# Optimization experiments

Hardware: AMD Instinct MI355X
Metric: run time of the kernel (lower is better)

Reference implementation:

```python
import jax, jax.numpy as jnp
import numpy as np

N, L, G = 8192, 120, 256          # sentences, seq_len, bags
V, P = 80000, 202                 # word vocab, position vocab
WDIM, FDIM = 50, 5                # word_size, feature_size (width = 50+2*5 = 60)
D, C = 230, 53                    # cnn_layers, num_classes


def setup_inputs() -> dict:
    key = jax.random.key(0)
    ks = jax.random.split(key, 9)
    x = jax.random.randint(ks[0], (N, L), 0, V, dtype=jnp.int32)
    ldist = jax.random.randint(ks[1], (N, L), 0, P, dtype=jnp.int32)
    rdist = jax.random.randint(ks[2], (N, L), 0, P, dtype=jnp.int32)
    # cumulative bag boundaries: 256 equal bags of 32 sentences
    total_shape = (jnp.arange(G + 1, dtype=jnp.int32) * (N // G))
    Wv = jax.random.normal(ks[3], (V, WDIM), dtype=jnp.float32) * 0.1
    pf1 = jax.random.normal(ks[4], (P, FDIM), dtype=jnp.float32) * 0.1
    pf2 = jax.random.normal(ks[5], (P, FDIM), dtype=jnp.float32) * 0.1
    Wc = jax.random.normal(ks[6], (D, 1, 3, WDIM + 2 * FDIM), dtype=jnp.float32) * 0.05
    bc = jnp.zeros((D,), dtype=jnp.float32)
    Wr = jax.random.normal(ks[7], (C, D), dtype=jnp.float32) * 0.05
    br = jnp.zeros((C,), dtype=jnp.float32)
    return dict(x=x, ldist=ldist, rdist=rdist, total_shape=total_shape,
                Wv=Wv, pf1=pf1, pf2=pf2, Wc=Wc, bc=bc, Wr=Wr, br=br)


def reference(x, ldist, rdist, total_shape, Wv, pf1, pf2, Wc, bc, Wr, br):
    n = x.shape[0]
    g = total_shape.shape[0] - 1
    # getEmbeddings: concat word + two position embeddings -> (N, L, 60)
    emb = jnp.concatenate([Wv[x], pf1[ldist], pf2[rdist]], axis=-1)
    # Conv2d(1, D, (3, 60)), VALID -> (N, D, L-2, 1)
    conv = jax.lax.conv_general_dilated(
        emb[:, None, :, :], Wc, window_strides=(1, 1), padding='VALID',
        dimension_numbers=('NCHW', 'OIHW', 'NCHW')) + bc[None, :, None, None]
    # max over positions, squeeze; dropout is identity at eval; tanh
    sent = jnp.tanh(jnp.max(conv, axis=2)[:, :, 0])           # (N, D)
    e = sent @ Wr.T + br                                       # (N, C) batch_e
    # ragged per-bag softmax over sentences (per class), honoring total_shape
    seg = jnp.searchsorted(total_shape, jnp.arange(n), side='right') - 1  # (N,)
    m = jax.ops.segment_max(e, seg, num_segments=g)            # (G, C)
    ex = jnp.exp(e - m[seg])
    den = jax.ops.segment_sum(ex, seg, num_segments=g)
    alpha = ex / den[seg]                                      # (N, C)
    # bag_rep[g, c, :] = sum_i alpha[i, c] * sent[i, :]
    bag = jax.ops.segment_sum(alpha[:, :, None] * sent[:, None, :], seg,
                              num_segments=g)                  # (G, C, D)
    scores = jnp.einsum('gcd,kd->gck', bag, Wr) + br           # (G, C, C)
    probs = jax.nn.softmax(scores, axis=-1)
    return jnp.diagonal(probs, axis1=1, axis2=2)               # (G, C)
```

## Files before the change

### kernel.cpp

```cpp
#include <hip/hip_runtime.h>
#include <hip/hip_bf16.h>

typedef __bf16 bf16x8 __attribute__((ext_vector_type(8)));
typedef float f32x16 __attribute__((ext_vector_type(16)));
typedef unsigned short ushort_t;

#define NSENT 8192
#define LSEQ  120
#define GBAGS 256
#define WDIM_ 50
#define DFILT 230
#define NCLS  53
#define KSTEPS 12
#define BFRAG_ELEMS (24*256*8)
#define LROWS 130
#define SPB 4

static __device__ __forceinline__ ushort_t f2bf(float f) {
    unsigned int u = __float_as_uint(f);
    unsigned int lsb = (u >> 16) & 1u;
    u += 0x7fffu + lsb;
    return (ushort_t)(u >> 16);
}

__global__ __launch_bounds__(256) void pcnn_prep_b(const float* __restrict__ Wc,
                                                   ushort_t* __restrict__ Bfrag) {
    int idx = blockIdx.x * 256 + threadIdx.x;
    if (idx >= BFRAG_ELEMS) return;
    int c   = idx >> 11;
    int rem = idx & 2047;
    int d   = rem >> 3;
    int j   = rem & 7;
    int k   = c * 8 + j;
    int dh  = k >> 6;
    int w   = k & 63;
    float val = (d < DFILT && w < 60) ? Wc[(d * 3 + dh) * 60 + w] : 0.0f;
    Bfrag[idx] = f2bf(val);
}

__device__ __forceinline__ void conv_gather(unsigned char* __restrict__ buf, int n,
    const int* __restrict__ x, const int* __restrict__ ld, const int* __restrict__ rd,
    const float* __restrict__ Wv, const float* __restrict__ pf1, const float* __restrict__ pf2,
    int tid) {
    if (tid >= 240) return;
    int l = tid >> 1, h = tid & 1;
    int tok = x[n * LSEQ + l];
    float v[32];
    const float* wr = Wv + tok * WDIM_;
    if (h == 0) {
        #pragma unroll
        for (int j = 0; j < 16; ++j) {
            float2 t2 = *reinterpret_cast<const float2*>(wr + 2 * j);
            v[2 * j] = t2.x; v[2 * j + 1] = t2.y;
        }
    } else {
        #pragma unroll
        for (int j = 0; j < 9; ++j) {
            float2 t2 = *reinterpret_cast<const float2*>(wr + 32 + 2 * j);
            v[2 * j] = t2.x; v[2 * j + 1] = t2.y;
        }
        int lp = ld[n * LSEQ + l], rp = rd[n * LSEQ + l];
        #pragma unroll
        for (int j = 0; j < 5; ++j) v[18 + j] = pf1[lp * 5 + j];
        #pragma unroll
        for (int j = 0; j < 5; ++j) v[23 + j] = pf2[rp * 5 + j];
        v[28] = v[29] = v[30] = v[31] = 0.0f;
    }
    #pragma unroll
    for (int ch = 0; ch < 4; ++ch) {
        ushort_t u8[8];
        #pragma unroll
        for (int j = 0; j < 8; ++j) u8[j] = f2bf(v[ch * 8 + j]);
        int w0 = h * 32 + ch * 8;
        int byteoff = l * 128 + ((w0 * 2) ^ ((l & 7) << 4));
        *reinterpret_cast<uint4*>(buf + byteoff) = *reinterpret_cast<const uint4*>(u8);
    }
}

__device__ __forceinline__ void conv_compute(const unsigned char* __restrict__ buf, int n,
    const bf16x8 (&Bf)[2][KSTEPS], const float* __restrict__ bc, float* __restrict__ sent,
    int wv, int lhalf, int l31) {
    float dmax0 = -1e30f, dmax1 = -1e30f;
    #pragma unroll
    for (int tt = 0; tt < 4; ++tt) {
        f32x16 acc0, acc1;
        #pragma unroll
        for (int r = 0; r < 16; ++r) { acc0[r] = 0.0f; acc1[r] = 0.0f; }
        int trow = tt * 32 + l31;
        #pragma unroll
        for (int ks = 0; ks < KSTEPS; ++ks) {
            int dh = ks >> 2, q = ks & 3;
            int l = trow + dh;
            int w0 = q * 16 + lhalf * 8;
            int byteoff = l * 128 + ((w0 * 2) ^ ((l & 7) << 4));
            bf16x8 Af = *reinterpret_cast<const bf16x8*>(buf + byteoff);
            acc0 = __builtin_amdgcn_mfma_f32_32x32x16_bf16(Af, Bf[0][ks], acc0, 0, 0, 0);
            acc1 = __builtin_amdgcn_mfma_f32_32x32x16_bf16(Af, Bf[1][ks], acc1, 0, 0, 0);
        }
        #pragma unroll
        for (int r = 0; r < 16; ++r) {
            int t = tt * 32 + (r & 3) + 8 * (r >> 2) + 4 * lhalf;
            bool valid = (tt < 3) || (t < LSEQ - 2);
            if (valid) { dmax0 = fmaxf(dmax0, acc0[r]); dmax1 = fmaxf(dmax1, acc1[r]); }
        }
    }
    dmax0 = fmaxf(dmax0, __shfl_xor(dmax0, 32));
    dmax1 = fmaxf(dmax1, __shfl_xor(dmax1, 32));
    if (lhalf == 0) {
        int d0 = (wv * 2 + 0) * 32 + l31;
        int d1 = (wv * 2 + 1) * 32 + l31;
        if (d0 < DFILT) sent[n * DFILT + d0] = tanhf(dmax0 + bc[d0]);
        if (d1 < DFILT) sent[n * DFILT + d1] = tanhf(dmax1 + bc[d1]);
    }
}

__global__ __launch_bounds__(256) void pcnn_conv_sent(
    const int* __restrict__ x, const int* __restrict__ ld, const int* __restrict__ rd,
    const float* __restrict__ Wv, const float* __restrict__ pf1, const float* __restrict__ pf2,
    const ushort_t* __restrict__ Bfrag, const float* __restrict__ bc,
    float* __restrict__ sent) {

    __shared__ __align__(16) unsigned char sembA[LROWS * 128];
    __shared__ __align__(16) unsigned char sembB[LROWS * 128];

    const int n0   = blockIdx.x * SPB;
    const int tid  = threadIdx.x;
    const int wv   = tid >> 6;
    const int lane = tid & 63;
    const int lhalf = lane >> 5;
    const int l31   = lane & 31;

    bf16x8 Bf[2][KSTEPS];
    #pragma unroll
    for (int i = 0; i < 2; ++i) {
        int dcol = (wv * 2 + i) * 32 + l31;
        #pragma unroll
        for (int ks = 0; ks < KSTEPS; ++ks) {
            int c = ks * 2 + lhalf;
            Bf[i][ks] = *reinterpret_cast<const bf16x8*>(Bfrag + ((c * 256 + dcol) << 3));
        }
    }

    if (tid < 160) {
        int b = tid / 80, j = tid % 80;
        unsigned char* base = (b == 0 ? sembA : sembB) + 120 * 128;
        reinterpret_cast<uint4*>(base)[j] = uint4{0, 0, 0, 0};
    }
    conv_gather(sembA, n0 + 0, x, ld, rd, Wv, pf1, pf2, tid);
    __syncthreads();

    conv_gather(sembB, n0 + 1, x, ld, rd, Wv, pf1, pf2, tid);
    conv_compute(sembA, n0 + 0, Bf, bc, sent, wv, lhalf, l31);
    __syncthreads();
    conv_gather(sembA, n0 + 2, x, ld, rd, Wv, pf1, pf2, tid);
    conv_compute(sembB, n0 + 1, Bf, bc, sent, wv, lhalf, l31);
    __syncthreads();
    conv_gather(sembB, n0 + 3, x, ld, rd, Wv, pf1, pf2, tid);
    conv_compute(sembA, n0 + 2, Bf, bc, sent, wv, lhalf, l31);
    __syncthreads();
    conv_compute(sembB, n0 + 3, Bf, bc, sent, wv, lhalf, l31);
}

#define MAXNS 32
#define CPAD 56
__global__ __launch_bounds__(256) void pcnn_bag(
    const float* __restrict__ sent, const float* __restrict__ Wr, const float* __restrict__ br,
    const int* __restrict__ tshape, float* __restrict__ out) {

    __shared__ float s_sent[MAXNS * DFILT];
    __shared__ float s_Wr[NCLS * DFILT];
    __shared__ float s_e[MAXNS * CPAD];
    __shared__ float s_alpha[MAXNS * CPAD];
    __shared__ float s_sc[NCLS * NCLS];
    __shared__ float s_br[CPAD];

    const int g = blockIdx.x;
    const int tid = threadIdx.x;
    int start = tshape[g], end = tshape[g + 1];
    int ns = end - start;
    if (ns > MAXNS) ns = MAXNS;

    {
        int n2 = ns * (DFILT / 2);
        const float2* src = reinterpret_cast<const float2*>(sent + start * DFILT);
        for (int idx = tid; idx < n2; idx += 256)
            reinterpret_cast<float2*>(s_sent)[idx] = src[idx];
        const float2* wsrc = reinterpret_cast<const float2*>(Wr);
        for (int idx = tid; idx < (NCLS * DFILT) / 2; idx += 256)
            reinterpret_cast<float2*>(s_Wr)[idx] = wsrc[idx];
        if (tid < NCLS) s_br[tid] = br[tid];
    }
    __syncthreads();

    if (tid < 224) {
        int i0 = tid / 14, c0 = tid % 14;
        float a00 = 0, a01 = 0, a02 = 0, a03 = 0;
        float a10 = 0, a11 = 0, a12 = 0, a13 = 0;
        const float* s0p = s_sent + (2 * i0) * DFILT;
        const float* s1p = s_sent + (2 * i0 + 1) * DFILT;
        const float* w0p = s_Wr + (4 * c0 + 0) * DFILT;
        const float* w1p = s_Wr + (4 * c0 + 1) * DFILT;
        const float* w2p = (4 * c0 + 2 < NCLS) ? s_Wr + (4 * c0 + 2) * DFILT : s_Wr;
        const float* w3p = (4 * c0 + 3 < NCLS) ? s_Wr + (4 * c0 + 3) * DFILT : s_Wr;
        for (int d = 0; d < DFILT; ++d) {
            float s0 = s0p[d], s1 = s1p[d];
            float w0 = w0p[d], w1 = w1p[d], w2 = w2p[d], w3 = w3p[d];
            a00 = fmaf(s0, w0, a00); a01 = fmaf(s0, w1, a01);
            a02 = fmaf(s0, w2, a02); a03 = fmaf(s0, w3, a03);
            a10 = fmaf(s1, w0, a10); a11 = fmaf(s1, w1, a11);
            a12 = fmaf(s1, w2, a12); a13 = fmaf(s1, w3, a13);
        }
        float av[2][4] = {{a00, a01, a02, a03}, {a10, a11, a12, a13}};
        #pragma unroll
        for (int ii = 0; ii < 2; ++ii) {
            int i = 2 * i0 + ii;
            #pragma unroll
            for (int j = 0; j < 4; ++j) {
                int c = 4 * c0 + j;
                if (i < ns && c < NCLS) s_e[i * CPAD + c] = av[ii][j] + s_br[c];
            }
        }
    }
    __syncthreads();

    if (tid < NCLS) {
        int c = tid;
        float m = -1e30f;
        for (int i = 0; i < ns; ++i) m = fmaxf(m, s_e[i * CPAD + c]);
        float den = 0.0f;
        for (int i = 0; i < ns; ++i) {
            float ex = expf(s_e[i * CPAD + c] - m);
            s_alpha[i * CPAD + c] = ex;
            den += ex;
        }
        float inv = 1.0f / den;
        for (int i = 0; i < ns; ++i) s_alpha[i * CPAD + c] *= inv;
    }
    __syncthreads();

    for (int task = tid; task < NCLS * 14; task += 256) {
        int c = task / 14, k0 = (task % 14) * 4;
        float b0 = s_br[k0], b1 = (k0+1<NCLS)?s_br[k0+1]:0.f, b2 = (k0+2<NCLS)?s_br[k0+2]:0.f, b3 = (k0+3<NCLS)?s_br[k0+3]:0.f;
        float a0 = 0, a1 = 0, a2 = 0, a3 = 0;
        for (int i = 0; i < ns; ++i) {
            float al = s_alpha[i * CPAD + c];
            const float* ep = s_e + i * CPAD + k0;
            a0 = fmaf(al, ep[0] - b0, a0);
            a1 = fmaf(al, (k0+1<NCLS?ep[1]:0.f) - b1, a1);
            a2 = fmaf(al, (k0+2<NCLS?ep[2]:0.f) - b2, a2);
            a3 = fmaf(al, (k0+3<NCLS?ep[3]:0.f) - b3, a3);
        }
        if (k0 + 0 < NCLS) s_sc[c * NCLS + k0 + 0] = a0 + b0;
        if (k0 + 1 < NCLS) s_sc[c * NCLS + k0 + 1] = a1 + b1;
        if (k0 + 2 < NCLS) s_sc[c * NCLS + k0 + 2] = a2 + b2;
        if (k0 + 3 < NCLS) s_sc[c * NCLS + k0 + 3] = a3 + b3;
    }
    __syncthreads();

    if (tid < NCLS) {
        int c = tid;
        float m = -1e30f;
        for (int k = 0; k < NCLS; ++k) m = fmaxf(m, s_sc[c * NCLS + k]);
        float den = 0.0f;
        for (int k = 0; k < NCLS; ++k) den += expf(s_sc[c * NCLS + k] - m);
        out[g * NCLS + c] = expf(s_sc[c * NCLS + c] - m) / den;
    }
}

extern "C" void kernel_launch(void* const* d_in, const int* in_sizes, int n_in,
                              void* d_out, int out_size, void* d_ws, size_t ws_size,
                              hipStream_t stream) {
    const int*   x   = (const int*)d_in[0];
    const int*   ldi = (const int*)d_in[1];
    const int*   rdi = (const int*)d_in[2];
    const int*   ts  = (const int*)d_in[3];
    const float* Wv  = (const float*)d_in[4];
    const float* pf1 = (const float*)d_in[5];
    const float* pf2 = (const float*)d_in[6];
    const float* Wc  = (const float*)d_in[7];
    const float* bc  = (const float*)d_in[8];
    const float* Wr  = (const float*)d_in[9];
    const float* br  = (const float*)d_in[10];
    float* out = (float*)d_out;

    ushort_t* Bfrag = (ushort_t*)d_ws;
    float* sent = (float*)((char*)d_ws + BFRAG_ELEMS * sizeof(ushort_t));

    pcnn_prep_b<<<(BFRAG_ELEMS + 255) / 256, 256, 0, stream>>>(Wc, Bfrag);
    pcnn_conv_sent<<<NSENT / SPB, 256, 0, stream>>>(x, ldi, rdi, Wv, pf1, pf2, Bfrag, bc, sent);
    pcnn_bag<<<GBAGS, 256, 0, stream>>>(sent, Wr, br, ts, out);
}
```

Before: 150.5 us.

## Pre-convert embedding tables to padded bf16 and simplify conv gather to single buffer

Adds a prep kernel that converts the full word-embedding table (80000x50 fp32) into a 64-wide padded bf16 table, and converts the position tables to bf16. The conv gather then copies 16-byte chunks straight into shared memory with no per-element conversion. This halves gathered bytes and spreads the gather over all 256 threads. The double-buffered gather/compute overlap is replaced with a single buffer and two barriers per sentence. The cost is converting the entire 16 MB vocab table (about 10 MB written) on every call, even though only the looked-up rows (about 1M tokens, roughly 200 MB of gathers) are needed.

```diff
diff --git a/kernel.cpp b/kernel.cpp
--- a/kernel.cpp
+++ b/kernel.cpp
@@ -16,6 +16,12 @@
 #define LROWS 130
 #define SPB 4
 
+#define OFF_BFRAG 0
+#define OFF_WV64  196608
+#define OFF_PF1B  (196608 + 10240000)
+#define OFF_PF2B  (OFF_PF1B + 2048)
+#define OFF_SENT  (OFF_PF2B + 2048)
+
 static __device__ __forceinline__ ushort_t f2bf(float f) {
     unsigned int u = __float_as_uint(f);
     unsigned int lsb = (u >> 16) & 1u;
@@ -24,8 +30,14 @@
 }
 
 __global__ __launch_bounds__(256) void pcnn_prep_b(const float* __restrict__ Wc,
-                                                   ushort_t* __restrict__ Bfrag) {
+                                                   const float* __restrict__ pf1,
+                                                   const float* __restrict__ pf2,
+                                                   ushort_t* __restrict__ Bfrag,
+                                                   ushort_t* __restrict__ pf1b,
+                                                   ushort_t* __restrict__ pf2b) {
     int idx = blockIdx.x * 256 + threadIdx.x;
+    if (idx < 1010) pf1b[idx] = f2bf(pf1[idx]);
+    else if (idx < 2020) pf2b[idx - 1010] = f2bf(pf2[idx - 1010]);
     if (idx >= BFRAG_ELEMS) return;
     int c   = idx >> 11;
     int rem = idx & 2047;
@@ -38,42 +50,45 @@
     Bfrag[idx] = f2bf(val);
 }
 
+__global__ __launch_bounds__(256) void pcnn_prep_wv(const float* __restrict__ Wv,
+                                                    ushort_t* __restrict__ Wv64) {
+    int idx = blockIdx.x * 256 + threadIdx.x;
+    int r = idx >> 6, k = idx & 63;
+    float val = (k < WDIM_) ? Wv[r * WDIM_ + k] : 0.0f;
+    Wv64[idx] = f2bf(val);
+}
+
 __device__ __forceinline__ void conv_gather(unsigned char* __restrict__ buf, int n,
     const int* __restrict__ x, const int* __restrict__ ld, const int* __restrict__ rd,
-    const float* __restrict__ Wv, const float* __restrict__ pf1, const float* __restrict__ pf2,
-    int tid) {
-    if (tid >= 240) return;
-    int l = tid >> 1, h = tid & 1;
-    int tok = x[n * LSEQ + l];
-    float v[32];
-    const float* wr = Wv + tok * WDIM_;
-    if (h == 0) {
-        #pragma unroll
-        for (int j = 0; j < 16; ++j) {
-            float2 t2 = *reinterpret_cast<const float2*>(wr + 2 * j);
-            v[2 * j] = t2.x; v[2 * j + 1] = t2.y;
-        }
-    } else {
-        #pragma unroll
-        for (int j = 0; j < 9; ++j) {
-            float2 t2 = *reinterpret_cast<const float2*>(wr + 32 + 2 * j);
-            v[2 * j] = t2.x; v[2 * j + 1] = t2.y;
-        }
-        int lp = ld[n * LSEQ + l], rp = rd[n * LSEQ + l];
-        #pragma unroll
-        for (int j = 0; j < 5; ++j) v[18 + j] = pf1[lp * 5 + j];
-        #pragma unroll
-        for (int j = 0; j < 5; ++j) v[23 + j] = pf2[rp * 5 + j];
-        v[28] = v[29] = v[30] = v[31] = 0.0f;
-    }
+    const ushort_t* __restrict__ Wv64, const ushort_t* __restrict__ pf1b,
+    const ushort_t* __restrict__ pf2b, int tid) {
     #pragma unroll
-    for (int ch = 0; ch < 4; ++ch) {
-        ushort_t u8[8];
-        #pragma unroll
-        for (int j = 0; j < 8; ++j) u8[j] = f2bf(v[ch * 8 + j]);
-        int w0 = h * 32 + ch * 8;
-        int byteoff = l * 128 + ((w0 * 2) ^ ((l & 7) << 4));
-        *reinterpret_cast<uint4*>(buf + byteoff) = *reinterpret_cast<const uint4*>(u8);
+    for (int j = 0; j < 4; ++j) {
+        int task = tid + 256 * j;
+        if (task >= LSEQ * 8) break;
+        int l = task >> 3, c = task & 7;
+        int tok = x[n * LSEQ + l];
+        int byteoff = l * 128 + (((c * 16)) ^ ((l & 7) << 4));
+        if (c < 6) {
+            *reinterpret_cast<uint4*>(buf + byteoff) =
+                *reinterpret_cast<const uint4*>(Wv64 + tok * 64 + c * 8);
+        } else if (c == 6) {
+            int lp = ld[n * LSEQ + l], rp = rd[n * LSEQ + l];
+            ushort_t u[8];
+            *reinterpret_cast<unsigned int*>(&u[0]) =
+                *reinterpret_cast<const unsigned int*>(Wv64 + tok * 64 + 48);
+            u[2] = pf1b[lp * 5 + 0]; u[3] = pf1b[lp * 5 + 1]; u[4] = pf1b[lp * 5 + 2];
+            u[5] = pf1b[lp * 5 + 3]; u[6] = pf1b[lp * 5 + 4];
+            u[7] = pf2b[rp * 5 + 0];
+            *reinterpret_cast<uint4*>(buf + byteoff) = *reinterpret_cast<const uint4*>(u);
+        } else {
+            int rp = rd[n * LSEQ + l];
+            ushort_t u[8];
+            u[0] = pf2b[rp * 5 + 1]; u[1] = pf2b[rp * 5 + 2];
+            u[2] = pf2b[rp * 5 + 3]; u[3] = pf2b[rp * 5 + 4];
+            u[4] = 0; u[5] = 0; u[6] = 0; u[7] = 0;
+            *reinterpret_cast<uint4*>(buf + byteoff) = *reinterpret_cast<const uint4*>(u);
+        }
     }
 }
 
@@ -116,12 +131,12 @@
 
 __global__ __launch_bounds__(256) void pcnn_conv_sent(
     const int* __restrict__ x, const int* __restrict__ ld, const int* __restrict__ rd,
-    const float* __restrict__ Wv, const float* __restrict__ pf1, const float* __restrict__ pf2,
+    const ushort_t* __restrict__ Wv64, const ushort_t* __restrict__ pf1b,
+    const ushort_t* __restrict__ pf2b,
     const ushort_t* __restrict__ Bfrag, const float* __restrict__ bc,
     float* __restrict__ sent) {
 
-    __shared__ __align__(16) unsigned char sembA[LROWS * 128];
-    __shared__ __align__(16) unsigned char sembB[LROWS * 128];
+    __shared__ __align__(16) unsigned char semb[LROWS * 128];
 
     const int n0   = blockIdx.x * SPB;
     const int tid  = threadIdx.x;
@@ -141,24 +156,15 @@
         }
     }
 
-    if (tid < 160) {
-        int b = tid / 80, j = tid % 80;
-        unsigned char* base = (b == 0 ? sembA : sembB) + 120 * 128;
-        reinterpret_cast<uint4*>(base)[j] = uint4{0, 0, 0, 0};
-    }
-    conv_gather(sembA, n0 + 0, x, ld, rd, Wv, pf1, pf2, tid);
-    __syncthreads();
-
-    conv_gather(sembB, n0 + 1, x, ld, rd, Wv, pf1, pf2, tid);
-    conv_compute(sembA, n0 + 0, Bf, bc, sent, wv, lhalf, l31);
-    __syncthreads();
-    conv_gather(sembA, n0 + 2, x, ld, rd, Wv, pf1, pf2, tid);
-    conv_compute(sembB, n0 + 1, Bf, bc, sent, wv, lhalf, l31);
-    __syncthreads();
-    conv_gather(sembB, n0 + 3, x, ld, rd, Wv, pf1, pf2, tid);
-    conv_compute(sembA, n0 + 2, Bf, bc, sent, wv, lhalf, l31);
-    __syncthreads();
-    conv_compute(sembB, n0 + 3, Bf, bc, sent, wv, lhalf, l31);
+    if (tid < 80) reinterpret_cast<uint4*>(semb + 120 * 128)[tid] = uint4{0, 0, 0, 0};
+
+    #pragma unroll
+    for (int s = 0; s < SPB; ++s) {
+        conv_gather(semb, n0 + s, x, ld, rd, Wv64, pf1b, pf2b, tid);
+        __syncthreads();
+        conv_compute(semb, n0 + s, Bf, bc, sent, wv, lhalf, l31);
+        __syncthreads();
+    }
 }
 
 #define MAXNS 32
@@ -215,9 +221,9 @@
         for (int ii = 0; ii < 2; ++ii) {
             int i = 2 * i0 + ii;
             #pragma unroll
-            for (int j = 0; j < 4; ++j) {
-                int c = 4 * c0 + j;
-                if (i < ns && c < NCLS) s_e[i * CPAD + c] = av[ii][j] + s_br[c];
+            for (int jj = 0; jj < 4; ++jj) {
+                int c = 4 * c0 + jj;
+                if (i < ns && c < NCLS) s_e[i * CPAD + c] = av[ii][jj] + s_br[c];
             }
         }
     }
@@ -283,10 +289,15 @@
     const float* br  = (const float*)d_in[10];
     float* out = (float*)d_out;
 
-    ushort_t* Bfrag = (ushort_t*)d_ws;
-    float* sent = (float*)((char*)d_ws + BFRAG_ELEMS * sizeof(ushort_t));
-
-    pcnn_prep_b<<<(BFRAG_ELEMS + 255) / 256, 256, 0, stream>>>(Wc, Bfrag);
-    pcnn_conv_sent<<<NSENT / SPB, 256, 0, stream>>>(x, ldi, rdi, Wv, pf1, pf2, Bfrag, bc, sent);
+    char* ws = (char*)d_ws;
+    ushort_t* Bfrag = (ushort_t*)(ws + OFF_BFRAG);
+    ushort_t* Wv64  = (ushort_t*)(ws + OFF_WV64);
+    ushort_t* pf1b  = (ushort_t*)(ws + OFF_PF1B);
+    ushort_t* pf2b  = (ushort_t*)(ws + OFF_PF2B);
+    float*    sent  = (float*)(ws + OFF_SENT);
+
+    pcnn_prep_b<<<(BFRAG_ELEMS + 255) / 256, 256, 0, stream>>>(Wc, pf1, pf2, Bfrag, pf1b, pf2b);
+    pcnn_prep_wv<<<(80000 * 64) / 256, 256, 0, stream>>>(Wv, Wv64);
+    pcnn_conv_sent<<<NSENT / SPB, 256, 0, stream>>>(x, ldi, rdi, Wv64, pf1b, pf2b, Bfrag, bc, sent);
     pcnn_bag<<<GBAGS, 256, 0, stream>>>(sent, Wr, br, ts, out);
 }
```

After: 202.9 us. 1.35x slower.
